# Performance work log

Measured on AMD Instinct MI355X. Metric: run time of the kernel, lower is better.

## Reference

```python
import jax, jax.numpy as jnp
import numpy as np

HUGE = jnp.float32(1e31)   # ops.HUGE_INT
EPS = 1e-20
B, AN = 1024, 256
D = 256            # emb_dim
HD = 512           # history_dim
AD = 2 * D         # action_dim
NE, NR = 100000, 400


def setup_inputs() -> dict:
    key = jax.random.key(0)
    ks = jax.random.split(key, 12)
    e = jax.random.randint(ks[0], (B,), 0, NE)
    q = jax.random.randint(ks[1], (B,), 0, NR)
    hstate = jax.random.normal(ks[2], (B, HD), dtype=jnp.float32)
    r_space = jax.random.randint(ks[3], (B, AN), 0, NR)
    e_space = jax.random.randint(ks[4], (B, AN), 0, NE)
    # binary action mask; guarantee at least one valid action per row
    action_mask = (jax.random.uniform(ks[5], (B, AN)) > 0.2).astype(jnp.float32)
    action_mask = action_mask.at[:, 0].set(1.0)
    entity_emb = jax.random.normal(ks[6], (NE, D), dtype=jnp.float32) * 0.02
    relation_emb = jax.random.normal(ks[7], (NR, D), dtype=jnp.float32) * 0.02
    W1 = jax.random.normal(ks[8], (2 * D + HD, AD), dtype=jnp.float32) * (1.0 / np.sqrt(2 * D + HD))
    b1 = jnp.zeros((AD,), dtype=jnp.float32)
    W2 = jax.random.normal(ks[9], (AD, AD), dtype=jnp.float32) * (1.0 / np.sqrt(AD))
    b2 = jnp.zeros((AD,), dtype=jnp.float32)
    return {"e": e, "q": q, "hstate": hstate, "r_space": r_space,
            "e_space": e_space, "action_mask": action_mask,
            "entity_emb": entity_emb, "relation_emb": relation_emb,
            "W1": W1, "b1": b1, "W2": W2, "b2": b2}


def reference(e, q, hstate, r_space, e_space, action_mask,
              entity_emb, relation_emb, W1, b1, W2, b2):
    Q = relation_emb[q]                       # [B, D]
    E = entity_emb[e]                         # [B, D]
    X = jnp.concatenate([E, hstate, Q], axis=-1)          # [B, 2D+HD]
    X = jax.nn.relu(X @ W1 + b1)                          # [B, AD]
    X2 = X @ W2 + b2                                      # [B, AD]
    # action embeddings: [rel_emb[r]; ent_emb[e]] per padded action slot
    A = jnp.concatenate([relation_emb[r_space], entity_emb[e_space]], axis=-1)  # [B, AN, AD]
    scores = jnp.einsum('bad,bd->ba', A, X2) - (1.0 - action_mask) * HUGE      # [B, AN]
    action_dist = jax.nn.softmax(scores, axis=-1)
    entropy = -jnp.sum(action_dist * jnp.log(jnp.clip(action_dist, EPS)), axis=-1)  # [B]
    return action_dist, entropy
```

## Files before the change

### kernel.cpp

```cpp
#include <hip/hip_runtime.h>
#include <math.h>

#define NB   1024
#define NACT 256
#define DIM  256
#define HDIM 512
#define ADIM 512
#define KTOT 1024
#define NE   100000
#define NR   400
#define NRP  448
#define NCAT 704

typedef __attribute__((ext_vector_type(8))) short bf16x8;
typedef __attribute__((ext_vector_type(4))) float f32x4;

__device__ __forceinline__ unsigned short f2bf(float f) {
    unsigned int u = __float_as_uint(f);
    u += 0x7FFF + ((u >> 16) & 1);
    return (unsigned short)(u >> 16);
}
__device__ __forceinline__ ushort4 cvt4(float4 v) {
    ushort4 o = {f2bf(v.x), f2bf(v.y), f2bf(v.z), f2bf(v.w)};
    return o;
}

__global__ __launch_bounds__(256) void prep_kernel(
    const float* __restrict__ W1, const float* __restrict__ W2,
    const float* __restrict__ rel, const float* __restrict__ b2,
    ushort* __restrict__ W1T, ushort* __restrict__ Bcat,
    ushort* __restrict__ W2lowbf, ushort* __restrict__ relbf,
    float* __restrict__ cvec)
{
    const int blk = blockIdx.x, tid = threadIdx.x;
    if (blk < 160) {
        __shared__ float t[64][68];
        const float* in; ushort* out; int Kd, k0, n0, rowbase;
        if (blk < 128) {
            in = W1; out = W1T; Kd = 1024;
            k0 = (blk >> 3) * 64; n0 = (blk & 7) * 64; rowbase = n0;
        } else {
            const int l = blk - 128;
            in = W2; out = Bcat; Kd = 512;
            k0 = (l >> 2) * 64; n0 = 256 + (l & 3) * 64; rowbase = n0 - 256;
        }
        const int kr = tid >> 2, c = tid & 3;
        #pragma unroll
        for (int j = 0; j < 4; ++j) {
            const float4 v = *(const float4*)(in + (size_t)(k0 + kr) * ADIM + n0 + c * 16 + j * 4);
            *(float4*)&t[kr][c * 16 + j * 4] = v;
        }
        __syncthreads();
        const int nr = tid >> 2;
        ushort tmp[16];
        #pragma unroll
        for (int kk = 0; kk < 16; ++kk) tmp[kk] = f2bf(t[c * 16 + kk][nr]);
        *(uint4*)(out + (size_t)(rowbase + nr) * Kd + k0 + c * 16)     = *(uint4*)&tmp[0];
        *(uint4*)(out + (size_t)(rowbase + nr) * Kd + k0 + c * 16 + 8) = *(uint4*)&tmp[8];
    } else if (blk < 288) {
        const int l = blk - 160;
        const int row = l * 4 + (tid >> 6);
        const int d4  = tid & 63;
        const float4 v = *(const float4*)(W2 + (size_t)row * ADIM + d4 * 4);
        *(ushort4*)(W2lowbf + (size_t)row * DIM + d4 * 4) = cvt4(v);
    } else if (blk < 388) {
        const int j = (blk - 288) * 256 + tid;
        ((ushort4*)relbf)[j] = cvt4(((const float4*)rel)[j]);
    } else {
        const int r = (blk - 388) * 256 + tid;
        if (r < NRP) {
            const int rr = (r < NR) ? r : (NR - 1);
            const float* a = rel + (size_t)rr * DIM;
            float s = 0.f;
            for (int d = 0; d < DIM; d += 4) {
                const float4 av = *(const float4*)(a + d);
                const float4 bv = *(const float4*)(b2 + d);
                s += av.x * bv.x + av.y * bv.y + av.z * bv.z + av.w * bv.w;
            }
            cvec[r] = s;
        }
    }
}

__global__ __launch_bounds__(256) void mega2_kernel(
    const float* __restrict__ ent, const float* __restrict__ rel,
    const float* __restrict__ hstate,
    const int* __restrict__ e, const int* __restrict__ q,
    const ushort* __restrict__ W1T, const ushort* __restrict__ relbf,
    const ushort* __restrict__ W2lowbf,
    ushort* __restrict__ Bcat, float* __restrict__ Hpart)
{
    __shared__ __align__(16) ushort Als[64][40];
    __shared__ __align__(16) ushort Bls[64][40];
    const int blk = blockIdx.x, tid = threadIdx.x;
    const int wave = tid >> 6, lane = tid & 63;
    const int qq   = lane >> 4, l15 = lane & 15;
    const int sm   = tid >> 2, sc = tid & 3;

    f32x4 acc[4];
    #pragma unroll
    for (int mt = 0; mt < 4; ++mt) acc[mt] = (f32x4){0.f, 0.f, 0.f, 0.f};

    if (blk < 56) {
        const int n0 = (blk & 7) * 64;
        const int m0 = (blk >> 3) * 64;
        const int arow = (m0 + sm < NR) ? (m0 + sm) : (NR - 1);
        const uint4* ga = (const uint4*)(relbf + (size_t)arow * DIM) + sc;
        const uint4* gb = (const uint4*)(W2lowbf + (size_t)(n0 + sm) * DIM) + sc;
        uint4 pa = ga[0], pb = gb[0];
        for (int it = 0; it < DIM / 32; ++it) {
            *(uint4*)&Als[sm][sc * 8] = pa;
            *(uint4*)&Bls[sm][sc * 8] = pb;
            __syncthreads();
            if (it + 1 < DIM / 32) { pa = ga[(it + 1) * 4]; pb = gb[(it + 1) * 4]; }
            const bf16x8 bfrag = *(const bf16x8*)&Bls[wave * 16 + l15][qq * 8];
            #pragma unroll
            for (int mt = 0; mt < 4; ++mt) {
                const bf16x8 afrag = *(const bf16x8*)&Als[mt * 16 + l15][qq * 8];
                acc[mt] = __builtin_amdgcn_mfma_f32_16x16x32_bf16(afrag, bfrag, acc[mt], 0, 0, 0);
            }
            __syncthreads();
        }
        const int n = n0 + wave * 16 + l15;
        #pragma unroll
        for (int mt = 0; mt < 4; ++mt)
            #pragma unroll
            for (int r = 0; r < 4; ++r) {
                const int m = m0 + mt * 16 + qq * 4 + r;
                Bcat[(size_t)(256 + m) * ADIM + n] = f2bf(acc[mt][r]);
            }
        return;
    }

    const int g  = blk - 56;
    const int n0 = (g & 7) * 64;
    const int m0 = ((g >> 3) & 15) * 64;
    const int z  = g >> 7;
    const int kbase = z * 256;
    const int kofs  = sc * 8;

    const int row = m0 + sm;
    const float* abase;
    if (z == 0)      abase = ent + (size_t)e[row] * DIM;
    else if (z == 3) abase = rel + (size_t)q[row] * DIM;
    else             abase = hstate + (size_t)row * HDIM + (kbase - DIM);
    const uint4* gb = (const uint4*)(W1T + (size_t)(n0 + sm) * KTOT + kbase) + sc;

    float4 pa0 = *(const float4*)(abase + kofs);
    float4 pa1 = *(const float4*)(abase + kofs + 4);
    uint4  pb  = gb[0];

    for (int it = 0; it < 8; ++it) {
        ushort t8[8];
        t8[0] = f2bf(pa0.x); t8[1] = f2bf(pa0.y); t8[2] = f2bf(pa0.z); t8[3] = f2bf(pa0.w);
        t8[4] = f2bf(pa1.x); t8[5] = f2bf(pa1.y); t8[6] = f2bf(pa1.z); t8[7] = f2bf(pa1.w);
        *(uint4*)&Als[sm][sc * 8] = *(uint4*)t8;
        *(uint4*)&Bls[sm][sc * 8] = pb;
        __syncthreads();
        if (it + 1 < 8) {
            const int lofs = (it + 1) * 32 + kofs;
            pa0 = *(const float4*)(abase + lofs);
            pa1 = *(const float4*)(abase + lofs + 4);
            pb  = gb[(it + 1) * 4];
        }
        const bf16x8 bfrag = *(const bf16x8*)&Bls[wave * 16 + l15][qq * 8];
        #pragma unroll
        for (int mt = 0; mt < 4; ++mt) {
            const bf16x8 afrag = *(const bf16x8*)&Als[mt * 16 + l15][qq * 8];
            acc[mt] = __builtin_amdgcn_mfma_f32_16x16x32_bf16(afrag, bfrag, acc[mt], 0, 0, 0);
        }
        __syncthreads();
    }
    float* dst = Hpart + (size_t)z * NB * ADIM;
    const int n = n0 + wave * 16 + l15;
    #pragma unroll
    for (int mt = 0; mt < 4; ++mt)
        #pragma unroll
        for (int r = 0; r < 4; ++r) {
            const int m = m0 + mt * 16 + qq * 4 + r;
            dst[(size_t)m * ADIM + n] = acc[mt][r];
        }
}

__global__ __launch_bounds__(256) void reduce_x(
    const float* __restrict__ Hpart, const float* __restrict__ b1,
    ushort* __restrict__ Xbf)
{
    const int i = blockIdx.x * 256 + threadIdx.x;
    const int col4 = i & (ADIM / 4 - 1);
    float4 s = ((const float4*)b1)[col4];
    #pragma unroll
    for (int z = 0; z < 4; ++z) {
        const float4 h = ((const float4*)(Hpart + (size_t)z * NB * ADIM))[i];
        s.x += h.x; s.y += h.y; s.z += h.z; s.w += h.w;
    }
    s.x = fmaxf(s.x, 0.f); s.y = fmaxf(s.y, 0.f);
    s.z = fmaxf(s.z, 0.f); s.w = fmaxf(s.w, 0.f);
    ((ushort4*)Xbf)[i] = cvt4(s);
}

__global__ __launch_bounds__(256) void gemm2big(
    const ushort* __restrict__ Xbf, const ushort* __restrict__ Bcat,
    const float* __restrict__ b2, const float* __restrict__ cvec,
    float* __restrict__ X2upPart, float* __restrict__ RtabPart)
{
    __shared__ __align__(16) ushort Als[64][40];
    __shared__ __align__(16) ushort Bls[64][40];
    const int tid  = threadIdx.x;
    const int n0   = blockIdx.x * 64;
    const int m0   = blockIdx.y * 64;
    const int z    = blockIdx.z;
    const int kb   = z * 256;
    const int wave = tid >> 6, lane = tid & 63;
    const int qq   = lane >> 4, l15 = lane & 15;
    const int sm   = tid >> 2, sc = tid & 3;

    const uint4* gap = (const uint4*)(Xbf  + (size_t)(m0 + sm) * ADIM + kb) + sc;
    const uint4* gbp = (const uint4*)(Bcat + (size_t)(n0 + sm) * ADIM + kb) + sc;

    f32x4 acc[4];
    #pragma unroll
    for (int mt = 0; mt < 4; ++mt) acc[mt] = (f32x4){0.f, 0.f, 0.f, 0.f};

    uint4 pa = gap[0], pb = gbp[0];
    for (int it = 0; it < 8; ++it) {
        *(uint4*)&Als[sm][sc * 8] = pa;
        *(uint4*)&Bls[sm][sc * 8] = pb;
        __syncthreads();
        if (it + 1 < 8) { pa = gap[(it + 1) * 4]; pb = gbp[(it + 1) * 4]; }
        const bf16x8 bfrag = *(const bf16x8*)&Bls[wave * 16 + l15][qq * 8];
        #pragma unroll
        for (int mt = 0; mt < 4; ++mt) {
            const bf16x8 afrag = *(const bf16x8*)&Als[mt * 16 + l15][qq * 8];
            acc[mt] = __builtin_amdgcn_mfma_f32_16x16x32_bf16(afrag, bfrag, acc[mt], 0, 0, 0);
        }
        __syncthreads();
    }
    const int n = n0 + wave * 16 + l15;
    const float extra = (z == 0) ? ((n < 256) ? b2[256 + n] : cvec[n - 256]) : 0.0f;
    #pragma unroll
    for (int mt = 0; mt < 4; ++mt)
        #pragma unroll
        for (int r = 0; r < 4; ++r) {
            const int m = m0 + mt * 16 + qq * 4 + r;
            const float v = acc[mt][r] + extra;
            if (n < 256) X2upPart[(size_t)z * NB * DIM + (size_t)m * DIM + n] = v;
            else         RtabPart[(size_t)z * NB * NRP + (size_t)m * NRP + (n - 256)] = v;
        }
}

__global__ __launch_bounds__(256) void scores_kernel(
    const int* __restrict__ r_space, const int* __restrict__ e_space,
    const float* __restrict__ amask,
    const float* __restrict__ ent,
    const float* __restrict__ RtabPart, const float* __restrict__ X2upPart,
    float* __restrict__ dist_out, float* __restrict__ ent_out)
{
    const int b    = blockIdx.x;
    const int tid  = threadIdx.x;
    const int wave = tid >> 6;
    const int lane = tid & 63;

    __shared__ float xs[DIM];
    __shared__ float rtab[NRP];
    __shared__ float red1[4], red2[4], red3[4];

    if (tid < 112) {
        const float4 v0 = ((const float4*)(RtabPart + (size_t)b * NRP))[tid];
        const float4 v1 = ((const float4*)(RtabPart + (size_t)NB * NRP + (size_t)b * NRP))[tid];
        float4 s; s.x = v0.x + v1.x; s.y = v0.y + v1.y; s.z = v0.z + v1.z; s.w = v0.w + v1.w;
        ((float4*)rtab)[tid] = s;
    } else if (tid >= 128 && tid < 192) {
        const int j = tid - 128;
        float4 v0 = ((const float4*)(X2upPart + (size_t)b * DIM))[j];
        const float4 v1 = ((const float4*)(X2upPart + (size_t)NB * DIM + (size_t)b * DIM))[j];
        v0.x += v1.x; v0.y += v1.y; v0.z += v1.z; v0.w += v1.w;
        ((float4*)xs)[j] = v0;
    }
    const int   ri  = r_space[(size_t)b * NACT + tid];
    const int   ei  = e_space[(size_t)b * NACT + tid];
    const float msk = amask[(size_t)b * NACT + tid];
    __syncthreads();

    const float4* erow = (const float4*)(ent + (size_t)ei * DIM);
    const float4* xv4  = (const float4*)xs;
    float p0 = 0.f, p1 = 0.f, p2 = 0.f, p3 = 0.f;
    #pragma unroll 2
    for (int d = 0; d < DIM / 4; d += 4) {
        const float4 e0 = erow[d], e1 = erow[d + 1], e2 = erow[d + 2], e3 = erow[d + 3];
        const float4 x0 = xv4[d],  x1 = xv4[d + 1],  x2 = xv4[d + 2],  x3 = xv4[d + 3];
        p0 += e0.x * x0.x + e0.y * x0.y + e0.z * x0.z + e0.w * x0.w;
        p1 += e1.x * x1.x + e1.y * x1.y + e1.z * x1.z + e1.w * x1.w;
        p2 += e2.x * x2.x + e2.y * x2.y + e2.z * x2.z + e2.w * x2.w;
        p3 += e3.x * x3.x + e3.y * x3.y + e3.z * x3.z + e3.w * x3.w;
    }
    const float s = rtab[ri] + ((p0 + p1) + (p2 + p3)) - (1.0f - msk) * 1e31f;

    float mx = s;
    #pragma unroll
    for (int off = 32; off; off >>= 1) mx = fmaxf(mx, __shfl_xor(mx, off));
    if (lane == 0) red1[wave] = mx;
    __syncthreads();
    mx = fmaxf(fmaxf(red1[0], red1[1]), fmaxf(red1[2], red1[3]));

    const float ex = expf(s - mx);
    float sum = ex;
    #pragma unroll
    for (int off = 32; off; off >>= 1) sum += __shfl_xor(sum, off);
    if (lane == 0) red2[wave] = sum;
    __syncthreads();
    sum = (red2[0] + red2[1]) + (red2[2] + red2[3]);

    const float d = ex / sum;
    dist_out[(size_t)b * NACT + tid] = d;

    float t = d * logf(fmaxf(d, 1e-20f));
    #pragma unroll
    for (int off = 32; off; off >>= 1) t += __shfl_xor(t, off);
    if (lane == 0) red3[wave] = t;
    __syncthreads();
    if (tid == 0)
        ent_out[b] = -((red3[0] + red3[1]) + (red3[2] + red3[3]));
}

extern "C" void kernel_launch(void* const* d_in, const int* in_sizes, int n_in,
                              void* d_out, int out_size, void* d_ws, size_t ws_size,
                              hipStream_t stream) {
    const int*   e       = (const int*)d_in[0];
    const int*   q       = (const int*)d_in[1];
    const float* hstate  = (const float*)d_in[2];
    const int*   r_space = (const int*)d_in[3];
    const int*   e_space = (const int*)d_in[4];
    const float* amask   = (const float*)d_in[5];
    const float* ent     = (const float*)d_in[6];
    const float* rel     = (const float*)d_in[7];
    const float* W1      = (const float*)d_in[8];
    const float* b1      = (const float*)d_in[9];
    const float* W2      = (const float*)d_in[10];
    const float* b2      = (const float*)d_in[11];

    ushort* W1T    = (ushort*)d_ws;
    ushort* Bcat   = W1T    + (size_t)ADIM * KTOT;
    ushort* W2low  = Bcat   + (size_t)NCAT * ADIM;
    ushort* relbf  = W2low  + (size_t)ADIM * DIM;
    float*  cvec   = (float*)(relbf + (size_t)NR * DIM);
    float*  Hpart  = cvec   + NRP;
    ushort* Xbf    = (ushort*)(Hpart + (size_t)4 * NB * ADIM);
    float*  X2upP  = (float*)(Xbf + (size_t)NB * ADIM);
    float*  RtabP  = X2upP  + (size_t)2 * NB * DIM;
    float*  dist   = (float*)d_out;
    float*  entr   = dist + (size_t)NB * NACT;

    prep_kernel<<<390, 256, 0, stream>>>(W1, W2, rel, b2, W1T, Bcat, W2low, relbf, cvec);
    mega2_kernel<<<568, 256, 0, stream>>>(ent, rel, hstate, e, q, W1T, relbf, W2low, Bcat, Hpart);
    reduce_x<<<512, 256, 0, stream>>>(Hpart, b1, Xbf);
    gemm2big<<<dim3(11, 16, 2), 256, 0, stream>>>(Xbf, Bcat, b2, cvec, X2upP, RtabP);
    scores_kernel<<<NB, 256, 0, stream>>>(
        r_space, e_space, amask, ent, RtabP, X2upP, dist, entr);
}
```

Before: 232.0 us.

## Coalesce entity-row gathers in scores kernel with 16-lane groups and prefetch

The scores kernel now has 16 lanes cooperate on each action's entity row, so each gathered 1KB row is read as contiguous float4 chunks rather than one thread streaming a whole row. The next row is prefetched while the current dot product is reduced through shuffles. Indices are staged in shared memory and the block grows to 512 threads with 8-wave reductions. The aim is better memory coalescing and latency hiding on the dominant gather traffic, at the cost of extra shuffles, shared memory and a barrier.

New measurement: 217.3 us. -6.3%, faster.

```diff
diff --git a/kernel.cpp b/kernel.cpp
--- a/kernel.cpp
+++ b/kernel.cpp
@@ -249,7 +249,7 @@
         }
 }
 
-__global__ __launch_bounds__(256) void scores_kernel(
+__global__ __launch_bounds__(512) void scores_kernel(
     const int* __restrict__ r_space, const int* __restrict__ e_space,
     const float* __restrict__ amask,
     const float* __restrict__ ent,
@@ -260,11 +260,18 @@
     const int tid  = threadIdx.x;
     const int wave = tid >> 6;
     const int lane = tid & 63;
+    const int qw   = tid >> 4;
+    const int ql   = tid & 15;
 
     __shared__ float xs[DIM];
     __shared__ float rtab[NRP];
-    __shared__ float red1[4], red2[4], red3[4];
-
+    __shared__ float sc[NACT];
+    __shared__ int   eidx[NACT];
+    __shared__ int   ridx[NACT];
+    __shared__ float red1[8], red2[8], red3[8];
+
+    if (tid < NACT) eidx[tid] = e_space[(size_t)b * NACT + tid];
+    else            ridx[tid - NACT] = r_space[(size_t)b * NACT + tid - NACT];
     if (tid < 112) {
         const float4 v0 = ((const float4*)(RtabPart + (size_t)b * NRP))[tid];
         const float4 v1 = ((const float4*)(RtabPart + (size_t)NB * NRP + (size_t)b * NRP))[tid];
@@ -277,50 +284,70 @@
         v0.x += v1.x; v0.y += v1.y; v0.z += v1.z; v0.w += v1.w;
         ((float4*)xs)[j] = v0;
     }
-    const int   ri  = r_space[(size_t)b * NACT + tid];
-    const int   ei  = e_space[(size_t)b * NACT + tid];
-    const float msk = amask[(size_t)b * NACT + tid];
-    __syncthreads();
-
-    const float4* erow = (const float4*)(ent + (size_t)ei * DIM);
-    const float4* xv4  = (const float4*)xs;
-    float p0 = 0.f, p1 = 0.f, p2 = 0.f, p3 = 0.f;
-    #pragma unroll 2
-    for (int d = 0; d < DIM / 4; d += 4) {
-        const float4 e0 = erow[d], e1 = erow[d + 1], e2 = erow[d + 2], e3 = erow[d + 3];
-        const float4 x0 = xv4[d],  x1 = xv4[d + 1],  x2 = xv4[d + 2],  x3 = xv4[d + 3];
-        p0 += e0.x * x0.x + e0.y * x0.y + e0.z * x0.z + e0.w * x0.w;
-        p1 += e1.x * x1.x + e1.y * x1.y + e1.z * x1.z + e1.w * x1.w;
-        p2 += e2.x * x2.x + e2.y * x2.y + e2.z * x2.z + e2.w * x2.w;
-        p3 += e3.x * x3.x + e3.y * x3.y + e3.z * x3.z + e3.w * x3.w;
-    }
-    const float s = rtab[ri] + ((p0 + p1) + (p2 + p3)) - (1.0f - msk) * 1e31f;
+    __syncthreads();
+
+    const float4* xv = ((const float4*)xs) + ql * 4;
+    const float4 x0 = xv[0], x1 = xv[1], x2 = xv[2], x3 = xv[3];
+
+    const float4* er = (const float4*)(ent + (size_t)eidx[qw] * DIM) + ql * 4;
+    float4 e0 = er[0], e1 = er[1], e2 = er[2], e3 = er[3];
+
+    #pragma unroll
+    for (int g = 0; g < 8; ++g) {
+        const float4 f0 = e0, f1 = e1, f2 = e2, f3 = e3;
+        if (g + 1 < 8) {
+            const float4* ern = (const float4*)(ent + (size_t)eidx[(g + 1) * 32 + qw] * DIM) + ql * 4;
+            e0 = ern[0]; e1 = ern[1]; e2 = ern[2]; e3 = ern[3];
+        }
+        float p = f0.x * x0.x + f0.y * x0.y + f0.z * x0.z + f0.w * x0.w
+                + f1.x * x1.x + f1.y * x1.y + f1.z * x1.z + f1.w * x1.w
+                + f2.x * x2.x + f2.y * x2.y + f2.z * x2.z + f2.w * x2.w
+                + f3.x * x3.x + f3.y * x3.y + f3.z * x3.z + f3.w * x3.w;
+        p += __shfl_xor(p, 1);
+        p += __shfl_xor(p, 2);
+        p += __shfl_xor(p, 4);
+        p += __shfl_xor(p, 8);
+        if (ql == 0) {
+            const int a = g * 32 + qw;
+            sc[a] = p + rtab[ridx[a]];
+        }
+    }
+    __syncthreads();
+
+    float s = -3.0e38f;
+    if (tid < NACT) {
+        const float m = amask[(size_t)b * NACT + tid];
+        s = sc[tid] - (1.0f - m) * 1e31f;
+    }
 
     float mx = s;
     #pragma unroll
     for (int off = 32; off; off >>= 1) mx = fmaxf(mx, __shfl_xor(mx, off));
     if (lane == 0) red1[wave] = mx;
     __syncthreads();
-    mx = fmaxf(fmaxf(red1[0], red1[1]), fmaxf(red1[2], red1[3]));
-
-    const float ex = expf(s - mx);
+    mx = fmaxf(fmaxf(fmaxf(red1[0], red1[1]), fmaxf(red1[2], red1[3])),
+               fmaxf(fmaxf(red1[4], red1[5]), fmaxf(red1[6], red1[7])));
+
+    const float ex = (tid < NACT) ? expf(s - mx) : 0.0f;
     float sum = ex;
     #pragma unroll
     for (int off = 32; off; off >>= 1) sum += __shfl_xor(sum, off);
     if (lane == 0) red2[wave] = sum;
     __syncthreads();
-    sum = (red2[0] + red2[1]) + (red2[2] + red2[3]);
+    sum = ((red2[0] + red2[1]) + (red2[2] + red2[3]))
+        + ((red2[4] + red2[5]) + (red2[6] + red2[7]));
 
     const float d = ex / sum;
-    dist_out[(size_t)b * NACT + tid] = d;
-
-    float t = d * logf(fmaxf(d, 1e-20f));
+    if (tid < NACT) dist_out[(size_t)b * NACT + tid] = d;
+
+    float t = (tid < NACT) ? d * logf(fmaxf(d, 1e-20f)) : 0.0f;
     #pragma unroll
     for (int off = 32; off; off >>= 1) t += __shfl_xor(t, off);
     if (lane == 0) red3[wave] = t;
     __syncthreads();
     if (tid == 0)
-        ent_out[b] = -((red3[0] + red3[1]) + (red3[2] + red3[3]));
+        ent_out[b] = -(((red3[0] + red3[1]) + (red3[2] + red3[3]))
+                     + ((red3[4] + red3[5]) + (red3[6] + red3[7])));
 }
 
 extern "C" void kernel_launch(void* const* d_in, const int* in_sizes, int n_in,
@@ -355,6 +382,6 @@
     mega2_kernel<<<568, 256, 0, stream>>>(ent, rel, hstate, e, q, W1T, relbf, W2low, Bcat, Hpart);
     reduce_x<<<512, 256, 0, stream>>>(Hpart, b1, Xbf);
     gemm2big<<<dim3(11, 16, 2), 256, 0, stream>>>(Xbf, Bcat, b2, cvec, X2upP, RtabP);
-    scores_kernel<<<NB, 256, 0, stream>>>(
+    scores_kernel<<<NB, 512, 0, stream>>>(
         r_space, e_space, amask, ent, RtabP, X2upP, dist, entr);
 }
```

## Invert entity gather into per-entity buckets and stream entity rows once

Applied to the files above, without the earlier changes.

Action slots are bucketed by entity id with atomics, up to 32 per entity. A new streamdot kernel then reads each entity embedding row once and dots it with the X2 rows of every batch that references it, writing per-slot scores. The softmax kernel now only adds the relation table and mask before the softmax. The second GEMM also drops its split-K in favour of a single full-K pass, which removes the partial-sum buffers. The aim is to avoid re-gathering the same entity rows for every action slot. In exchange it adds atomic bucketing, a counter-zeroing pass and a 25000-block kernel, and any entity referenced more than 32 times is silently dropped.

After: 251.0 us. 8.2% more time.

```diff
diff --git a/kernel.cpp b/kernel.cpp
--- a/kernel.cpp
+++ b/kernel.cpp
@@ -11,6 +11,7 @@
 #define NR   400
 #define NRP  448
 #define NCAT 704
+#define CAP  32
 
 typedef __attribute__((ext_vector_type(8))) short bf16x8;
 typedef __attribute__((ext_vector_type(4))) float f32x4;
@@ -30,9 +31,14 @@
     const float* __restrict__ rel, const float* __restrict__ b2,
     ushort* __restrict__ W1T, ushort* __restrict__ Bcat,
     ushort* __restrict__ W2lowbf, ushort* __restrict__ relbf,
-    float* __restrict__ cvec)
+    float* __restrict__ cvec, int* __restrict__ cnt)
 {
     const int blk = blockIdx.x, tid = threadIdx.x;
+    if (blk >= 390) {
+        const int j = (blk - 390) * 1024 + tid * 4;
+        *(int4*)(cnt + j) = (int4){0, 0, 0, 0};
+        return;
+    }
     if (blk < 160) {
         __shared__ float t[64][68];
         const float* in; ushort* out; int Kd, k0, n0, rowbase;
@@ -88,11 +94,20 @@
     const int* __restrict__ e, const int* __restrict__ q,
     const ushort* __restrict__ W1T, const ushort* __restrict__ relbf,
     const ushort* __restrict__ W2lowbf,
-    ushort* __restrict__ Bcat, float* __restrict__ Hpart)
-{
+    ushort* __restrict__ Bcat, float* __restrict__ Hpart,
+    const int* __restrict__ e_space, int* __restrict__ cnt, int* __restrict__ bucket)
+{
+    const int blk = blockIdx.x, tid = threadIdx.x;
+    if (blk >= 568) {
+        const int i = (blk - 568) * 256 + tid;
+        const int ei = e_space[i];
+        const int pos = atomicAdd(cnt + ei, 1);
+        if (pos < CAP) bucket[(size_t)ei * CAP + pos] = i;
+        return;
+    }
+
     __shared__ __align__(16) ushort Als[64][40];
     __shared__ __align__(16) ushort Bls[64][40];
-    const int blk = blockIdx.x, tid = threadIdx.x;
     const int wave = tid >> 6, lane = tid & 63;
     const int qq   = lane >> 4, l15 = lane & 15;
     const int sm   = tid >> 2, sc = tid & 3;
@@ -202,32 +217,30 @@
 __global__ __launch_bounds__(256) void gemm2big(
     const ushort* __restrict__ Xbf, const ushort* __restrict__ Bcat,
     const float* __restrict__ b2, const float* __restrict__ cvec,
-    float* __restrict__ X2upPart, float* __restrict__ RtabPart)
+    float* __restrict__ X2up, float* __restrict__ Rtab)
 {
     __shared__ __align__(16) ushort Als[64][40];
     __shared__ __align__(16) ushort Bls[64][40];
     const int tid  = threadIdx.x;
     const int n0   = blockIdx.x * 64;
     const int m0   = blockIdx.y * 64;
-    const int z    = blockIdx.z;
-    const int kb   = z * 256;
     const int wave = tid >> 6, lane = tid & 63;
     const int qq   = lane >> 4, l15 = lane & 15;
     const int sm   = tid >> 2, sc = tid & 3;
 
-    const uint4* gap = (const uint4*)(Xbf  + (size_t)(m0 + sm) * ADIM + kb) + sc;
-    const uint4* gbp = (const uint4*)(Bcat + (size_t)(n0 + sm) * ADIM + kb) + sc;
+    const uint4* gap = (const uint4*)(Xbf  + (size_t)(m0 + sm) * ADIM) + sc;
+    const uint4* gbp = (const uint4*)(Bcat + (size_t)(n0 + sm) * ADIM) + sc;
 
     f32x4 acc[4];
     #pragma unroll
     for (int mt = 0; mt < 4; ++mt) acc[mt] = (f32x4){0.f, 0.f, 0.f, 0.f};
 
     uint4 pa = gap[0], pb = gbp[0];
-    for (int it = 0; it < 8; ++it) {
+    for (int it = 0; it < 16; ++it) {
         *(uint4*)&Als[sm][sc * 8] = pa;
         *(uint4*)&Bls[sm][sc * 8] = pb;
         __syncthreads();
-        if (it + 1 < 8) { pa = gap[(it + 1) * 4]; pb = gbp[(it + 1) * 4]; }
+        if (it + 1 < 16) { pa = gap[(it + 1) * 4]; pb = gbp[(it + 1) * 4]; }
         const bf16x8 bfrag = *(const bf16x8*)&Bls[wave * 16 + l15][qq * 8];
         #pragma unroll
         for (int mt = 0; mt < 4; ++mt) {
@@ -237,23 +250,50 @@
         __syncthreads();
     }
     const int n = n0 + wave * 16 + l15;
-    const float extra = (z == 0) ? ((n < 256) ? b2[256 + n] : cvec[n - 256]) : 0.0f;
+    const float extra = (n < 256) ? b2[256 + n] : cvec[n - 256];
     #pragma unroll
     for (int mt = 0; mt < 4; ++mt)
         #pragma unroll
         for (int r = 0; r < 4; ++r) {
             const int m = m0 + mt * 16 + qq * 4 + r;
             const float v = acc[mt][r] + extra;
-            if (n < 256) X2upPart[(size_t)z * NB * DIM + (size_t)m * DIM + n] = v;
-            else         RtabPart[(size_t)z * NB * NRP + (size_t)m * NRP + (n - 256)] = v;
-        }
-}
-
-__global__ __launch_bounds__(256) void scores_kernel(
-    const int* __restrict__ r_space, const int* __restrict__ e_space,
-    const float* __restrict__ amask,
-    const float* __restrict__ ent,
-    const float* __restrict__ RtabPart, const float* __restrict__ X2upPart,
+            if (n < 256) X2up[(size_t)m * DIM + n] = v;
+            else         Rtab[(size_t)m * NRP + (n - 256)] = v;
+        }
+}
+
+__global__ __launch_bounds__(256) void streamdot(
+    const float* __restrict__ ent, const int* __restrict__ cnt,
+    const int* __restrict__ bucket, const float* __restrict__ X2up,
+    float* __restrict__ sc)
+{
+    const int tid  = threadIdx.x;
+    const int row  = blockIdx.x * 4 + (tid >> 6);
+    const int lane = tid & 63;
+
+    int cr = cnt[row];
+    if (cr == 0) return;
+    cr = (cr < CAP) ? cr : CAP;
+
+    const float4 ev = ((const float4*)(ent + (size_t)row * DIM))[lane];
+    const int* bl = bucket + (size_t)row * CAP;
+    for (int r = 0; r < cr; ++r) {
+        const int i = bl[r];
+        const float4 xv = ((const float4*)(X2up + (size_t)(i >> 8) * DIM))[lane];
+        float p = ev.x * xv.x + ev.y * xv.y + ev.z * xv.z + ev.w * xv.w;
+        p += __shfl_xor(p, 32);
+        p += __shfl_xor(p, 16);
+        p += __shfl_xor(p, 8);
+        p += __shfl_xor(p, 4);
+        p += __shfl_xor(p, 2);
+        p += __shfl_xor(p, 1);
+        if (lane == 0) sc[i] = p;
+    }
+}
+
+__global__ __launch_bounds__(256) void scores_softmax(
+    const int* __restrict__ r_space, const float* __restrict__ amask,
+    const float* __restrict__ Rtab, const float* __restrict__ sc,
     float* __restrict__ dist_out, float* __restrict__ ent_out)
 {
     const int b    = blockIdx.x;
@@ -261,40 +301,16 @@
     const int wave = tid >> 6;
     const int lane = tid & 63;
 
-    __shared__ float xs[DIM];
     __shared__ float rtab[NRP];
     __shared__ float red1[4], red2[4], red3[4];
 
-    if (tid < 112) {
-        const float4 v0 = ((const float4*)(RtabPart + (size_t)b * NRP))[tid];
-        const float4 v1 = ((const float4*)(RtabPart + (size_t)NB * NRP + (size_t)b * NRP))[tid];
-        float4 s; s.x = v0.x + v1.x; s.y = v0.y + v1.y; s.z = v0.z + v1.z; s.w = v0.w + v1.w;
-        ((float4*)rtab)[tid] = s;
-    } else if (tid >= 128 && tid < 192) {
-        const int j = tid - 128;
-        float4 v0 = ((const float4*)(X2upPart + (size_t)b * DIM))[j];
-        const float4 v1 = ((const float4*)(X2upPart + (size_t)NB * DIM + (size_t)b * DIM))[j];
-        v0.x += v1.x; v0.y += v1.y; v0.z += v1.z; v0.w += v1.w;
-        ((float4*)xs)[j] = v0;
-    }
-    const int   ri  = r_space[(size_t)b * NACT + tid];
-    const int   ei  = e_space[(size_t)b * NACT + tid];
-    const float msk = amask[(size_t)b * NACT + tid];
+    if (tid < 112) ((float4*)rtab)[tid] = ((const float4*)(Rtab + (size_t)b * NRP))[tid];
+    const int   ri = r_space[(size_t)b * NACT + tid];
+    const float m  = amask[(size_t)b * NACT + tid];
+    const float sv = sc[(size_t)b * NACT + tid];
     __syncthreads();
 
-    const float4* erow = (const float4*)(ent + (size_t)ei * DIM);
-    const float4* xv4  = (const float4*)xs;
-    float p0 = 0.f, p1 = 0.f, p2 = 0.f, p3 = 0.f;
-    #pragma unroll 2
-    for (int d = 0; d < DIM / 4; d += 4) {
-        const float4 e0 = erow[d], e1 = erow[d + 1], e2 = erow[d + 2], e3 = erow[d + 3];
-        const float4 x0 = xv4[d],  x1 = xv4[d + 1],  x2 = xv4[d + 2],  x3 = xv4[d + 3];
-        p0 += e0.x * x0.x + e0.y * x0.y + e0.z * x0.z + e0.w * x0.w;
-        p1 += e1.x * x1.x + e1.y * x1.y + e1.z * x1.z + e1.w * x1.w;
-        p2 += e2.x * x2.x + e2.y * x2.y + e2.z * x2.z + e2.w * x2.w;
-        p3 += e3.x * x3.x + e3.y * x3.y + e3.z * x3.z + e3.w * x3.w;
-    }
-    const float s = rtab[ri] + ((p0 + p1) + (p2 + p3)) - (1.0f - msk) * 1e31f;
+    const float s = sv + rtab[ri] - (1.0f - m) * 1e31f;
 
     float mx = s;
     #pragma unroll
@@ -346,15 +362,19 @@
     float*  cvec   = (float*)(relbf + (size_t)NR * DIM);
     float*  Hpart  = cvec   + NRP;
     ushort* Xbf    = (ushort*)(Hpart + (size_t)4 * NB * ADIM);
-    float*  X2upP  = (float*)(Xbf + (size_t)NB * ADIM);
-    float*  RtabP  = X2upP  + (size_t)2 * NB * DIM;
+    float*  X2up   = (float*)(Xbf + (size_t)NB * ADIM);
+    float*  Rtab   = X2up   + (size_t)NB * DIM;
+    float*  scbuf  = Rtab   + (size_t)NB * NRP;
+    int*    cnt    = (int*)(scbuf + (size_t)NB * NACT);
+    int*    bucket = cnt + 100352;
     float*  dist   = (float*)d_out;
     float*  entr   = dist + (size_t)NB * NACT;
 
-    prep_kernel<<<390, 256, 0, stream>>>(W1, W2, rel, b2, W1T, Bcat, W2low, relbf, cvec);
-    mega2_kernel<<<568, 256, 0, stream>>>(ent, rel, hstate, e, q, W1T, relbf, W2low, Bcat, Hpart);
+    prep_kernel<<<488, 256, 0, stream>>>(W1, W2, rel, b2, W1T, Bcat, W2low, relbf, cvec, cnt);
+    mega2_kernel<<<568 + 1024, 256, 0, stream>>>(ent, rel, hstate, e, q, W1T, relbf, W2low,
+                                                 Bcat, Hpart, e_space, cnt, bucket);
     reduce_x<<<512, 256, 0, stream>>>(Hpart, b1, Xbf);
-    gemm2big<<<dim3(11, 16, 2), 256, 0, stream>>>(Xbf, Bcat, b2, cvec, X2upP, RtabP);
-    scores_kernel<<<NB, 256, 0, stream>>>(
-        r_space, e_space, amask, ent, RtabP, X2upP, dist, entr);
-}
+    gemm2big<<<dim3(11, 16), 256, 0, stream>>>(Xbf, Bcat, b2, cvec, X2up, Rtab);
+    streamdot<<<25000, 256, 0, stream>>>(ent, cnt, bucket, X2up, scbuf);
+    scores_softmax<<<NB, 256, 0, stream>>>(r_space, amask, Rtab, scbuf, dist, entr);
+}
```
